# Optimization experiments

Hardware: AMD Instinct MI355X
Metric: run time of the kernel (lower is better)

Reference implementation:

```python
import jax, jax.numpy as jnp
import numpy as np

NUM_JOINTS = 21
IMG_SIZE = 256
RADIUS = IMG_SIZE // 2  # 128
G_SIZE = 11
G_SIGMA = 2.5


def _gaussian_kernel():
    # 2D gaussian, normalized to sum=1 then scaled so peak == 1 (peak_to_one=True)
    ax = np.arange(G_SIZE, dtype=np.float32) - (G_SIZE - 1) / 2.0
    g1 = np.exp(-(ax ** 2) / (2.0 * G_SIGMA ** 2))
    k = np.outer(g1, g1)
    k = k / k.sum()
    k = k / k.max()
    return jnp.asarray(k, dtype=jnp.float32)


def setup_inputs() -> dict:
    key = jax.random.key(0)
    joint = jax.random.normal(key, (64, NUM_JOINTS, 3), dtype=jnp.float32)
    return {"joint": joint}


def _convert_to_uv(joint):
    # equidistant fisheye projection: r = radius * theta / (pi/2)
    x, y, z = joint[..., 0], joint[..., 1], joint[..., 2]
    theta = jnp.arctan2(jnp.sqrt(x * x + y * y), z)
    phi = jnp.arctan2(y, x)
    r = RADIUS * theta / (jnp.pi / 2)
    fish_x = jnp.round(RADIUS + r * jnp.cos(phi))
    fish_y = jnpp_round = jnp.round(RADIUS + r * jnp.sin(phi))
    return jnp.stack([fish_x, fish_y], axis=-1)  # [B, J, 2]


def reference(joint):
    B, J = joint.shape[:2]
    uv = _convert_to_uv(joint)  # [B, J, 2] (x, y)
    # scatter one-hot heatmap seeds (GenHeatmapSeed)
    idx = jnp.clip(jnp.round(uv).astype(jnp.int32), 0, IMG_SIZE - 1)
    idx = idx.reshape(-1, 2)
    bj = jnp.arange(B * J)
    seeds = jnp.zeros((B * J, IMG_SIZE, IMG_SIZE), dtype=jnp.float32)
    seeds = seeds.at[bj, idx[:, 1], idx[:, 0]].set(1.0)
    seeds = seeds.reshape(B, J, IMG_SIZE, IMG_SIZE)
    # depthwise gaussian conv, SAME padding, peak-to-one kernel
    k2d = _gaussian_kernel()
    kernel = jnp.broadcast_to(k2d, (J, 1, G_SIZE, G_SIZE))  # OIHW depthwise
    heatmap = jax.lax.conv_general_dilated(
        seeds, kernel,
        window_strides=(1, 1), padding="SAME",
        dimension_numbers=("NCHW", "OIHW", "NCHW"),
        feature_group_count=J)
    return heatmap
```

## Files before the change

kernel.cpp:

```cpp
#include <hip/hip_runtime.h>
#include <math.h>

#define NUM_JOINTS 21
#define BATCH 64
#define BJ (BATCH * NUM_JOINTS)
#define IMG 256
#define IMG_PIX (IMG * IMG)
#define F4_PER_IMG (IMG_PIX / 4)

typedef float v4f __attribute__((ext_vector_type(4)));

__global__ void seed_kernel(const float* __restrict__ joint,
                            int2* __restrict__ seeds) {
    int i = blockIdx.x * blockDim.x + threadIdx.x;
    if (i >= BJ) return;
    float x = joint[i * 3 + 0];
    float y = joint[i * 3 + 1];
    float z = joint[i * 3 + 2];
    float theta = atan2f(sqrtf(x * x + y * y), z);
    float phi   = atan2f(y, x);
    float r = (128.0f * theta) / 1.5707964f;
    float fx = rintf(128.0f + r * cosf(phi));
    float fy = rintf(128.0f + r * sinf(phi));
    int sx = (int)fx;
    int sy = (int)fy;
    sx = min(max(sx, 0), IMG - 1);
    sy = min(max(sy, 0), IMG - 1);
    seeds[i] = make_int2(sx, sy);
}

__global__ void __launch_bounds__(256)
fill_kernel(const int2* __restrict__ seeds, float* __restrict__ out) {
    const unsigned total = BJ * F4_PER_IMG;
    const unsigned stride = gridDim.x * blockDim.x;
    for (unsigned idx = blockIdx.x * blockDim.x + threadIdx.x;
         idx < total; idx += stride) {
        unsigned img = idx >> 14;
        unsigned p   = (idx & (F4_PER_IMG - 1)) << 2;
        int h = p >> 8;
        int w = p & 255;

        int2 s = seeds[img];
        int dy = h - s.y;

        v4f v = (v4f)0.0f;
        if (dy >= -5 && dy <= 5) {
            int dx0 = w - s.x;
            if (dx0 <= 5 && dx0 >= -8) {
                float gy = expf(-(float)(dy * dy) / 12.5f);
                #pragma unroll
                for (int i = 0; i < 4; ++i) {
                    int dx = dx0 + i;
                    if (dx >= -5 && dx <= 5) {
                        v[i] = gy * expf(-(float)(dx * dx) / 12.5f);
                    }
                }
            }
        }

        v4f* dst = (v4f*)(out + (size_t)idx * 4);
        __builtin_nontemporal_store(v, dst);
    }
}

extern "C" void kernel_launch(void* const* d_in, const int* in_sizes, int n_in,
                              void* d_out, int out_size, void* d_ws, size_t ws_size,
                              hipStream_t stream) {
    const float* joint = (const float*)d_in[0];
    float* out = (float*)d_out;
    int2* seeds = (int2*)d_ws;

    seed_kernel<<<(BJ + 255) / 256, 256, 0, stream>>>(joint, seeds);

    fill_kernel<<<2048, 256, 0, stream>>>(seeds, out);
}
```

Measured before the change: 344.7 us.

## Zero output with memset and scatter only the Gaussian patch per image

The kernel that computed every output pixel is replaced. The whole output is now zeroed with hipMemsetAsync, and a small per-image kernel writes only the 11x11 Gaussian patch around each seed, using vector stores where a 4-wide chunk fits inside the image. This removes the per-pixel index and branch work and relies on the memset path running close to bandwidth. The risk is that out_size is taken as an element count; if it were a byte count, the memset would overrun the buffer.

```diff
diff --git a/kernel.cpp b/kernel.cpp
--- a/kernel.cpp
+++ b/kernel.cpp
@@ -6,7 +6,6 @@
 #define BJ (BATCH * NUM_JOINTS)
 #define IMG 256
 #define IMG_PIX (IMG * IMG)
-#define F4_PER_IMG (IMG_PIX / 4)
 
 typedef float v4f __attribute__((ext_vector_type(4)));
 
@@ -29,37 +28,38 @@
     seeds[i] = make_int2(sx, sy);
 }
 
-__global__ void __launch_bounds__(256)
-fill_kernel(const int2* __restrict__ seeds, float* __restrict__ out) {
-    const unsigned total = BJ * F4_PER_IMG;
-    const unsigned stride = gridDim.x * blockDim.x;
-    for (unsigned idx = blockIdx.x * blockDim.x + threadIdx.x;
-         idx < total; idx += stride) {
-        unsigned img = idx >> 14;
-        unsigned p   = (idx & (F4_PER_IMG - 1)) << 2;
-        int h = p >> 8;
-        int w = p & 255;
+__global__ void __launch_bounds__(64)
+patch_kernel(const int2* __restrict__ seeds, float* __restrict__ out) {
+    int img = blockIdx.x;
+    int t = threadIdx.x;
+    if (t >= 44) return;
+    int2 s = seeds[img];
+    int r = t >> 2;
+    int q = t & 3;
+    int y = s.y - 5 + r;
+    if (y < 0 || y > IMG - 1) return;
+    int dyy = r - 5;
+    float gy = expf(-(float)(dyy * dyy) / 12.5f);
 
-        int2 s = seeds[img];
-        int dy = h - s.y;
-
-        v4f v = (v4f)0.0f;
-        if (dy >= -5 && dy <= 5) {
-            int dx0 = w - s.x;
-            if (dx0 <= 5 && dx0 >= -8) {
-                float gy = expf(-(float)(dy * dy) / 12.5f);
-                #pragma unroll
-                for (int i = 0; i < 4; ++i) {
-                    int dx = dx0 + i;
-                    if (dx >= -5 && dx <= 5) {
-                        v[i] = gy * expf(-(float)(dx * dx) / 12.5f);
-                    }
-                }
-            }
+    int c0 = (s.x - 5) & ~3;
+    int cq = c0 + 4 * q;
+    float vals[4];
+    #pragma unroll
+    for (int i = 0; i < 4; ++i) {
+        int dx = cq + i - s.x;
+        vals[i] = (dx >= -5 && dx <= 5)
+                    ? gy * expf(-(float)(dx * dx) / 12.5f) : 0.0f;
+    }
+    float* row = out + (size_t)img * IMG_PIX + (size_t)y * IMG;
+    if (cq >= 0 && cq + 3 <= IMG - 1) {
+        v4f v = {vals[0], vals[1], vals[2], vals[3]};
+        *(v4f*)(row + cq) = v;
+    } else {
+        #pragma unroll
+        for (int i = 0; i < 4; ++i) {
+            int c = cq + i;
+            if (c >= 0 && c <= IMG - 1 && vals[i] != 0.0f) row[c] = vals[i];
         }
-
-        v4f* dst = (v4f*)(out + (size_t)idx * 4);
-        __builtin_nontemporal_store(v, dst);
     }
 }
 
@@ -70,7 +70,9 @@
     float* out = (float*)d_out;
     int2* seeds = (int2*)d_ws;
 
+    hipMemsetAsync(d_out, 0, (size_t)out_size * sizeof(float), stream);
+
     seed_kernel<<<(BJ + 255) / 256, 256, 0, stream>>>(joint, seeds);
 
-    fill_kernel<<<2048, 256, 0, stream>>>(seeds, out);
+    patch_kernel<<<BJ, 64, 0, stream>>>(seeds, out);
 }
```

Measured after the change: 342.5 us. No clear change (-0.6%).
